# Optimization experiments

Hardware: AMD Instinct MI355X
Metric: run time of the kernel (lower is better)

Reference implementation:

```python
import jax, jax.numpy as jnp
import numpy as np

B, S, H = 32, 512, 768
NHEAD, DH = 8, 96          # 8 heads * 96 = 768
E = 4096                   # edges per sample
NC = 2
NEG = -1e9
EPS = 1e-5


def _p(k, shape, scale=0.02):
    return scale * jax.random.normal(k, shape, dtype=jnp.float32)


def setup_inputs() -> dict:
    key = jax.random.key(0)
    ks = jax.random.split(key, 24)
    z = lambda *s: jnp.zeros(s, jnp.float32)
    return {
        "diff_encoded": jax.random.normal(ks[0], (B, S, H), jnp.float32),
        "msg_encoded": jax.random.normal(ks[1], (B, S, H), jnp.float32),
        "msg_mask": jnp.ones((B, S), jnp.int32),
        "edge_index_diff": jax.random.randint(ks[2], (B, 2, E), 0, S),
        "edge_index_msg": jax.random.randint(ks[3], (B, 2, E), 0, S),
        # GATv2Conv(heads=1): lin_l (source/message), lin_r (target), att vector, output bias
        "gat_wl": _p(ks[4], (H, H)), "gat_bl": z(H),
        "gat_wr": _p(ks[5], (H, H)), "gat_br": z(H),
        "gat_att": _p(ks[6], (H,)), "gat_bias": z(H),
        # cross MultiheadAttention
        "wq": _p(ks[7], (H, H)), "bq": z(H),
        "wk": _p(ks[8], (H, H)), "bk": z(H),
        "wv": _p(ks[9], (H, H)), "bv": z(H),
        "wo": _p(ks[10], (H, H)), "bo": z(H),
        # LayerNorm + MLP head
        "ln_g": jnp.ones((H,), jnp.float32), "ln_b": z(H),
        "fc0_w": _p(ks[11], (H, 512)), "fc0_b": z(512),
        "fc1_w": _p(ks[12], (512, 128)), "fc1_b": z(128),
        "fc2_w": _p(ks[13], (128, NC)), "fc2_b": z(NC),
    }


def _gat_single(x, edges, wl, bl, wr, br, att, bias):
    # GATv2Conv, heads=1, add_self_loops=True. x: [N,H], edges: [2,E] (src, dst).
    N = x.shape[0]
    src, dst = edges[0], edges[1]
    valid = (src < N) & (dst < N)            # clip_edge_index, as a mask
    src = jnp.where(valid, src, 0)
    dst = jnp.where(valid, dst, 0)
    loop = jnp.arange(N, dtype=src.dtype)    # PyG adds self loops
    src_a = jnp.concatenate([src, loop])
    dst_a = jnp.concatenate([dst, loop])
    valid_a = jnp.concatenate([valid, jnp.ones((N,), bool)])
    xl = x @ wl + bl                          # source / message transform
    xr = x @ wr + br                          # target transform
    e = jax.nn.leaky_relu(xl[src_a] + xr[dst_a], 0.2) @ att   # [E+N]
    e = jnp.where(valid_a, e, NEG)
    emax = jax.ops.segment_max(e, dst_a, num_segments=N)
    p = jnp.exp(e - emax[dst_a]) * valid_a.astype(x.dtype)
    denom = jax.ops.segment_sum(p, dst_a, num_segments=N)
    alpha = p / denom[dst_a]
    out = jax.ops.segment_sum(alpha[:, None] * xl[src_a], dst_a, num_segments=N)
    return out + bias


_gat = jax.vmap(_gat_single, in_axes=(0, 0) + (None,) * 6)


def _layernorm(x, g, b):
    mu = jnp.mean(x, -1, keepdims=True)
    var = jnp.mean(jnp.square(x - mu), -1, keepdims=True)
    return (x - mu) * jax.lax.rsqrt(var + EPS) * g + b


def reference(diff_encoded, msg_encoded, msg_mask, edge_index_diff, edge_index_msg,
              gat_wl, gat_bl, gat_wr, gat_br, gat_att, gat_bias,
              wq, bq, wk, bk, wv, bv, wo, bo, ln_g, ln_b,
              fc0_w, fc0_b, fc1_w, fc1_b, fc2_w, fc2_b):
    diff_g = _gat(diff_encoded, edge_index_diff, gat_wl, gat_bl, gat_wr, gat_br, gat_att, gat_bias) + diff_encoded
    msg_g = _gat(msg_encoded, edge_index_msg, gat_wl, gat_bl, gat_wr, gat_br, gat_att, gat_bias) + msg_encoded
    # cross attention: query=diff_g, key/value=msg_g, key_padding_mask = (msg_mask == 0)
    q = (diff_g @ wq + bq).reshape(B, S, NHEAD, DH)
    k = (msg_g @ wk + bk).reshape(B, S, NHEAD, DH)
    v = (msg_g @ wv + bv).reshape(B, S, NHEAD, DH)
    scores = jnp.einsum("bqhd,bkhd->bhqk", q, k) / jnp.sqrt(jnp.float32(DH))
    scores = jnp.where((msg_mask == 0)[:, None, None, :], NEG, scores)
    attn = jax.nn.softmax(scores, axis=-1)
    ctx = jnp.einsum("bhqk,bkhd->bqhd", attn, v).reshape(B, S, H) @ wo + bo
    fused = _layernorm(ctx + diff_g, ln_g, ln_b)
    x = fused[:, 0, :]                                  # CLS token
    x = jax.nn.relu(x @ fc0_w + fc0_b)                  # dropout = identity (eval)
    x = jax.nn.relu(x @ fc1_w + fc1_b)
    return x @ fc2_w + fc2_b
```

## Files before the change

kernel.cpp:

```cpp
#include <hip/hip_runtime.h>
#include <hip/hip_bf16.h>
#include <math.h>

#define BB 32
#define SS 512
#define HH 768
#define NHEADC 8
#define DHC 96
#define EE 4096
#define EAC (EE + SS)
#define NCC 2
#define CAPC 128
#define CAP2 32
#define GSL 36
#define XRS 1536
#define NEGV -1000000000.0f
#define EPSV 1e-5f

typedef __hip_bfloat16 bf16;
typedef __bf16 bf16x8 __attribute__((ext_vector_type(8)));
typedef float f32x4 __attribute__((ext_vector_type(4)));

static __device__ inline unsigned short f2bf_u(float f) {
  __hip_bfloat16 h = __float2bfloat16(f);
  return *(unsigned short*)&h;
}
static __device__ inline float bfu(unsigned short u) {
  return __uint_as_float(((unsigned int)u) << 16);
}
static __device__ inline float bf2f(bf16 h) { return __bfloat162float(h); }

static __device__ inline void gload16(const void* g, void* l) {
  __builtin_amdgcn_global_load_lds(
      (const __attribute__((address_space(1))) void*)g,
      (__attribute__((address_space(3))) void*)l, 16, 0, 0);
}

__global__ __launch_bounds__(256) void k_cvt_bf16(const float* __restrict__ x,
                                                  bf16* __restrict__ y, int n) {
  int i = (blockIdx.x * 256 + threadIdx.x) * 4;
  if (i >= n) return;
  float4 v = *(const float4*)(x + i);
  ushort4 o;
  o.x = f2bf_u(v.x); o.y = f2bf_u(v.y); o.z = f2bf_u(v.z); o.w = f2bf_u(v.w);
  *(ushort4*)((unsigned short*)y + i) = o;
}

__global__ __launch_bounds__(256) void k_cvt_wt(
    const float* __restrict__ w0, const float* __restrict__ w1,
    const float* __restrict__ w2, const float* __restrict__ w3,
    bf16* __restrict__ o0, bf16* __restrict__ o1,
    bf16* __restrict__ o2, bf16* __restrict__ o3) {
  const float* w; bf16* o;
  switch (blockIdx.z) {
    case 0: w = w0; o = o0; break;
    case 1: w = w1; o = o1; break;
    case 2: w = w2; o = o2; break;
    default: w = w3; o = o3; break;
  }
  __shared__ float t[32][33];
  int n0 = blockIdx.x * 32, k0 = blockIdx.y * 32;
  int x = threadIdx.x & 31, y = threadIdx.x >> 5;
  for (int yy = y; yy < 32; yy += 8)
    t[yy][x] = w[(size_t)(k0 + yy) * HH + n0 + x];
  __syncthreads();
  for (int yy = y; yy < 32; yy += 8)
    o[(size_t)(n0 + yy) * HH + k0 + x] = __float2bfloat16(t[x][yy]);
}

__global__ __launch_bounds__(256) void k_bias_stack(
    const float* __restrict__ bl, const float* __restrict__ br,
    const float* __restrict__ bk, const float* __restrict__ bv,
    float* __restrict__ biasA, float* __restrict__ biasB) {
  int t = blockIdx.x * 256 + threadIdx.x;
  if (t < HH) {
    biasA[t] = bl[t]; biasA[HH + t] = br[t];
    biasB[t] = bk[t]; biasB[HH + t] = bv[t];
  }
}

template <typename OT>
__global__ __launch_bounds__(256) void k_gemm(
    const bf16* __restrict__ A, const bf16* __restrict__ Bt,
    const float* __restrict__ bias, OT* __restrict__ C,
    int M, int N, int K, int ldc)
{
  __shared__ __align__(16) bf16 As[128 * 32];
  __shared__ __align__(16) bf16 Bs[128 * 32];
  const int tid = threadIdx.x;
  const int wv = tid >> 6, lane = tid & 63;
  const int bm = blockIdx.x * 128, bn = blockIdx.y * 128;
  const int wm = (wv & 1) * 64, wn = (wv >> 1) * 64;
  const int m16 = lane & 15, half = lane >> 4;
  f32x4 acc[4][4];
  #pragma unroll
  for (int i = 0; i < 4; ++i)
    #pragma unroll
    for (int j = 0; j < 4; ++j) acc[i][j] = (f32x4){0.f, 0.f, 0.f, 0.f};

  const int c0 = tid, c1 = tid + 256;
  const int r0 = c0 >> 2, o0 = (c0 & 3) * 8;
  const int r1 = c1 >> 2, o1 = (c1 & 3) * 8;
  const size_t aB0 = (size_t)(bm + r0) * K + o0;
  const size_t aB1 = (size_t)(bm + r1) * K + o1;
  const size_t bB0 = (size_t)(bn + r0) * K + o0;
  const size_t bB1 = (size_t)(bn + r1) * K + o1;

  for (int k0 = 0; k0 < K; k0 += 32) {
    __syncthreads();
    gload16(A + aB0 + k0, As + (size_t)c0 * 8);
    gload16(A + aB1 + k0, As + (size_t)c1 * 8);
    gload16(Bt + bB0 + k0, Bs + (size_t)c0 * 8);
    gload16(Bt + bB1 + k0, Bs + (size_t)c1 * 8);
    __syncthreads();
    bf16x8 af[4], bfv[4];
    #pragma unroll
    for (int t = 0; t < 4; ++t) {
      af[t]  = *(const bf16x8*)(As + (wm + t * 16 + m16) * 32 + half * 8);
      bfv[t] = *(const bf16x8*)(Bs + (wn + t * 16 + m16) * 32 + half * 8);
    }
    #pragma unroll
    for (int i = 0; i < 4; ++i)
      #pragma unroll
      for (int j = 0; j < 4; ++j)
        acc[i][j] = __builtin_amdgcn_mfma_f32_16x16x32_bf16(af[i], bfv[j], acc[i][j], 0, 0, 0);
  }
  #pragma unroll
  for (int i = 0; i < 4; ++i) {
    #pragma unroll
    for (int j = 0; j < 4; ++j) {
      int col = bn + wn + j * 16 + m16;
      float bv = bias ? bias[col] : 0.f;
      #pragma unroll
      for (int r = 0; r < 4; ++r) {
        int row = bm + wm + i * 16 + half * 4 + r;
        float v = acc[i][j][r] + bv;
        if constexpr (sizeof(OT) == 2)
          C[(size_t)row * ldc + col] = (OT)__float2bfloat16(v);
        else
          C[(size_t)row * ldc + col] = v;
      }
    }
  }
}

__global__ __launch_bounds__(256) void k_gat_edge(
    const int* __restrict__ eidx, const bf16* __restrict__ xlr,
    const float* __restrict__ att,
    float* __restrict__ evals, int* __restrict__ esrc, int* __restrict__ edst,
    int* __restrict__ cnt)
{
  int w = blockIdx.x * 4 + (threadIdx.x >> 6);
  int lane = threadIdx.x & 63;
  if (w >= BB * EAC) return;
  int b = w / EAC, j = w - b * EAC;
  int s, d; bool valid;
  if (j < EE) {
    s = eidx[b * 2 * EE + j];
    d = eidx[b * 2 * EE + EE + j];
    valid = (s >= 0 && s < SS && d >= 0 && d < SS);
    if (!valid) { s = 0; d = 0; }
  } else { s = j - EE; d = s; valid = true; }
  const ushort4* pl4 = (const ushort4*)(xlr + ((size_t)b * SS + s) * XRS);
  const ushort4* pr4 = (const ushort4*)(xlr + ((size_t)b * SS + d) * XRS + HH);
  const float4* a4 = (const float4*)att;
  float part = 0.f;
  #pragma unroll
  for (int r = 0; r < 3; ++r) {
    int c = lane + 64 * r;
    ushort4 vl = pl4[c];
    ushort4 vr = pr4[c];
    float4 av = a4[c];
    float t0 = bfu(vl.x) + bfu(vr.x);
    float t1 = bfu(vl.y) + bfu(vr.y);
    float t2 = bfu(vl.z) + bfu(vr.z);
    float t3 = bfu(vl.w) + bfu(vr.w);
    t0 = t0 > 0.f ? t0 : 0.2f * t0;
    t1 = t1 > 0.f ? t1 : 0.2f * t1;
    t2 = t2 > 0.f ? t2 : 0.2f * t2;
    t3 = t3 > 0.f ? t3 : 0.2f * t3;
    part += t0 * av.x + t1 * av.y + t2 * av.z + t3 * av.w;
  }
  #pragma unroll
  for (int off = 32; off > 0; off >>= 1) part += __shfl_xor(part, off);
  if (lane == 0) {
    evals[w] = valid ? part : NEGV;
    esrc[w] = s;
    edst[w] = d;
    atomicAdd(&cnt[b * SS + d], 1);
  }
}

__global__ __launch_bounds__(512) void k_scan(const int* __restrict__ cnt,
                                              int* __restrict__ offs,
                                              int* __restrict__ cursor) {
  __shared__ int tmp[SS];
  int b = blockIdx.x, t = threadIdx.x;
  int x = cnt[b * SS + t];
  tmp[t] = x;
  __syncthreads();
  for (int off = 1; off < SS; off <<= 1) {
    int u = (t >= off) ? tmp[t - off] : 0;
    __syncthreads();
    tmp[t] += u;
    __syncthreads();
  }
  int ex = tmp[t] - x;
  offs[b * SS + t] = ex;
  cursor[b * SS + t] = ex;
}

__global__ void k_scatter(const int* __restrict__ edst, int* __restrict__ cursor,
                          int* __restrict__ binned) {
  int i = blockIdx.x * blockDim.x + threadIdx.x;
  if (i >= BB * EAC) return;
  int b = i / EAC, j = i - b * EAC;
  int d = edst[i];
  int pos = atomicAdd(&cursor[b * SS + d], 1);
  binned[b * EAC + pos] = j;
}

__global__ __launch_bounds__(64) void k_gat_reduce(
    const float* __restrict__ evals, const int* __restrict__ esrc,
    const int* __restrict__ binned, const int* __restrict__ offs,
    const int* __restrict__ cnt, const bf16* __restrict__ xlr,
    const float* __restrict__ gbias, const float* __restrict__ resid,
    bf16* __restrict__ out)
{
  int b = blockIdx.x / SS, d = blockIdx.x % SS;
  int lane = threadIdx.x;
  int base = offs[b * SS + d], n = cnt[b * SS + d];
  const float* ev = evals + (size_t)b * EAC;
  const int* bb = binned + (size_t)b * EAC + base;
  float m = -3.0e38f;
  for (int i = lane; i < n; i += 64) m = fmaxf(m, ev[bb[i]]);
  #pragma unroll
  for (int off = 32; off > 0; off >>= 1) m = fmaxf(m, __shfl_xor(m, off));
  float ssum = 0.f;
  for (int i = lane; i < n; i += 64) ssum += expf(ev[bb[i]] - m);
  #pragma unroll
  for (int off = 32; off > 0; off >>= 1) ssum += __shfl_xor(ssum, off);
  float inv = 1.f / ssum;
  float acc[12] = {};
  for (int i = 0; i < n; ++i) {
    int j = bb[i];
    float a = expf(ev[j] - m) * inv;
    const ushort4* px4 =
        (const ushort4*)(xlr + ((size_t)b * SS + esrc[(size_t)b * EAC + j]) * XRS);
    #pragma unroll
    for (int r = 0; r < 3; ++r) {
      ushort4 v = px4[lane + 64 * r];
      acc[4 * r + 0] += a * bfu(v.x);
      acc[4 * r + 1] += a * bfu(v.y);
      acc[4 * r + 2] += a * bfu(v.z);
      acc[4 * r + 3] += a * bfu(v.w);
    }
  }
  size_t o = ((size_t)b * SS + d) * HH;
  const float4* gb4 = (const float4*)gbias;
  const float4* rs4 = (const float4*)(resid + o);
  ushort4* out4 = (ushort4*)(out + o);
  #pragma unroll
  for (int r = 0; r < 3; ++r) {
    int c = lane + 64 * r;
    float4 g = gb4[c], rr = rs4[c];
    ushort4 ov;
    ov.x = f2bf_u(acc[4 * r + 0] + g.x + rr.x);
    ov.y = f2bf_u(acc[4 * r + 1] + g.y + rr.y);
    ov.z = f2bf_u(acc[4 * r + 2] + g.z + rr.z);
    ov.w = f2bf_u(acc[4 * r + 3] + g.w + rr.w);
    out4[c] = ov;
  }
}

__global__ void k_diff_collect(const int* __restrict__ eidx, int* __restrict__ dcnt,
                               int* __restrict__ dsrc) {
  int i = blockIdx.x * blockDim.x + threadIdx.x;
  if (i >= BB * EAC) return;
  int b = i / EAC, j = i - b * EAC;
  int s, d; bool valid;
  if (j < EE) {
    s = eidx[b * 2 * EE + j];
    d = eidx[b * 2 * EE + EE + j];
    valid = (s >= 0 && s < SS && d >= 0 && d < SS);
  } else { s = j - EE; d = s; valid = true; }
  if (valid && d == 0) {
    int pos = atomicAdd(&dcnt[b], 1);
    if (pos < CAPC) dsrc[b * CAPC + pos] = s;
  }
}

__global__ __launch_bounds__(192) void k_gather_diff(
    const int* __restrict__ dcnt, const int* __restrict__ dsrc,
    const float* __restrict__ diff_enc, bf16* __restrict__ G)
{
  int b = blockIdx.y, jj = blockIdx.x;
  int n = min(dcnt[b], CAP2);
  int t = threadIdx.x;
  size_t orow = ((size_t)b * GSL + jj) * HH;
  ushort4 o = {0, 0, 0, 0};
  if (jj < n || jj == CAP2) {
    int s = (jj == CAP2) ? 0 : dsrc[b * CAPC + jj];
    float4 v = ((const float4*)(diff_enc + ((size_t)b * SS + s) * HH))[t];
    o.x = f2bf_u(v.x); o.y = f2bf_u(v.y); o.z = f2bf_u(v.z); o.w = f2bf_u(v.w);
  }
  *(ushort4*)((unsigned short*)G + orow + t * 4) = o;
}

__global__ __launch_bounds__(256) void k_diff_gat0(
    const int* __restrict__ dcnt, const float* __restrict__ GD,
    const float* __restrict__ att, const float* __restrict__ gbias,
    const float* __restrict__ diff_enc, float* __restrict__ dg0)
{
  int b = blockIdx.x;
  int n = min(dcnt[b], CAP2);
  __shared__ float ee[CAP2];
  __shared__ float al[CAP2];
  __shared__ float xr0s[HH];
  int wave = threadIdx.x >> 6, lane = threadIdx.x & 63;
  for (int h = threadIdx.x; h < HH; h += 256)
    xr0s[h] = GD[((size_t)b * GSL + CAP2) * XRS + HH + h];
  __syncthreads();
  for (int jj = wave; jj < n; jj += 4) {
    const float* px = GD + ((size_t)b * GSL + jj) * XRS;
    float part = 0.f;
    #pragma unroll
    for (int r = 0; r < HH / 64; ++r) {
      int h = lane + 64 * r;
      float t = px[h] + xr0s[h];
      t = t > 0.f ? t : 0.2f * t;
      part += t * att[h];
    }
    #pragma unroll
    for (int off = 32; off > 0; off >>= 1) part += __shfl_xor(part, off);
    if (lane == 0) ee[jj] = part;
  }
  __syncthreads();
  if (threadIdx.x == 0) {
    float m = -3.0e38f;
    for (int i = 0; i < n; ++i) m = fmaxf(m, ee[i]);
    float ssum = 0.f;
    for (int i = 0; i < n; ++i) ssum += expf(ee[i] - m);
    float inv = 1.f / ssum;
    for (int i = 0; i < n; ++i) al[i] = expf(ee[i] - m) * inv;
  }
  __syncthreads();
  for (int h = threadIdx.x; h < HH; h += 256) {
    float acc = 0.f;
    for (int i = 0; i < n; ++i) acc += al[i] * GD[((size_t)b * GSL + i) * XRS + h];
    dg0[b * HH + h] = acc + gbias[h] + diff_enc[(size_t)b * SS * HH + h];
  }
}

__global__ __launch_bounds__(256) void k_colmat(
    const float* __restrict__ in, const float* __restrict__ w,
    const float* __restrict__ bias, const float* __restrict__ extra,
    float* __restrict__ outp, int Kd, int Nd, long in_stride, int relu)
{
  int b = blockIdx.y, n0 = blockIdx.x * 64;
  int tid = threadIdx.x, wv = tid >> 6, lane = tid & 63;
  __shared__ float xs[HH];
  __shared__ float red[4][64];
  const float* src = in + (size_t)b * in_stride;
  for (int k = tid; k < Kd; k += 256) xs[k] = src[k];
  __syncthreads();
  int h = n0 + lane;
  int kpw = Kd >> 2;
  int kb = wv * kpw;
  float acc = 0.f;
  for (int k = 0; k < kpw; k += 8) {
    #pragma unroll
    for (int u = 0; u < 8; ++u) {
      int kk = kb + k + u;
      acc += xs[kk] * w[(size_t)kk * Nd + h];
    }
  }
  red[wv][lane] = acc;
  __syncthreads();
  if (tid < 64) {
    float s = red[0][tid] + red[1][tid] + red[2][tid] + red[3][tid] + bias[n0 + tid];
    if (extra) s += extra[(size_t)b * Nd + n0 + tid];
    if (relu) s = fmaxf(s, 0.f);
    outp[(size_t)b * Nd + n0 + tid] = s;
  }
}

__global__ __launch_bounds__(256) void k_ln(
    const float* __restrict__ xin, const float* __restrict__ g,
    const float* __restrict__ bta, float* __restrict__ yout)
{
  int b = blockIdx.x, tid = threadIdx.x;
  __shared__ float red[4], redq[4];
  float v0 = xin[b * HH + tid];
  float v1 = xin[b * HH + tid + 256];
  float v2 = xin[b * HH + tid + 512];
  float sum = v0 + v1 + v2;
  float sq = v0 * v0 + v1 * v1 + v2 * v2;
  #pragma unroll
  for (int off = 32; off > 0; off >>= 1) { sum += __shfl_xor(sum, off); sq += __shfl_xor(sq, off); }
  int wv = tid >> 6, lane = tid & 63;
  if (lane == 0) { red[wv] = sum; redq[wv] = sq; }
  __syncthreads();
  sum = red[0] + red[1] + red[2] + red[3];
  sq = redq[0] + redq[1] + redq[2] + redq[3];
  float mu = sum / HH;
  float var = sq / HH - mu * mu;
  float scl = rsqrtf(var + EPSV);
  yout[b * HH + tid]       = (v0 - mu) * scl * g[tid]       + bta[tid];
  yout[b * HH + tid + 256] = (v1 - mu) * scl * g[tid + 256] + bta[tid + 256];
  yout[b * HH + tid + 512] = (v2 - mu) * scl * g[tid + 512] + bta[tid + 512];
}

__global__ __launch_bounds__(256) void k_fc12(
    const float* __restrict__ a0g, const float* __restrict__ fc1w,
    const float* __restrict__ fc1b, const float* __restrict__ fc2w,
    const float* __restrict__ fc2b, float* __restrict__ out)
{
  int b = blockIdx.x, tid = threadIdx.x;
  __shared__ float a0s[512];
  __shared__ float a1s[128];
  __shared__ float r1[2][128];
  for (int k = tid; k < 512; k += 256) a0s[k] = a0g[b * 512 + k];
  __syncthreads();
  int o = tid & 127, hf = tid >> 7;
  int kb = hf * 256;
  float acc = 0.f;
  for (int k = 0; k < 256; k += 8) {
    #pragma unroll
    for (int u = 0; u < 8; ++u) {
      int kk = kb + k + u;
      acc += a0s[kk] * fc1w[(size_t)kk * 128 + o];
    }
  }
  r1[hf][o] = acc;
  __syncthreads();
  if (tid < 128) a1s[tid] = fmaxf(r1[0][tid] + r1[1][tid] + fc1b[tid], 0.f);
  __syncthreads();
  if (tid < 128) {
    int oo = tid >> 6, l = tid & 63;
    float p = a1s[l] * fc2w[l * 2 + oo] + a1s[l + 64] * fc2w[(l + 64) * 2 + oo];
    #pragma unroll
    for (int off = 32; off > 0; off >>= 1) p += __shfl_xor(p, off);
    if (l == 0) out[b * NCC + oo] = p + fc2b[oo];
  }
}

__global__ __launch_bounds__(512) void k_attn(
    const float* __restrict__ q0, const bf16* __restrict__ kvb,
    const int* __restrict__ mask, float* __restrict__ ctx)
{
  int b = blockIdx.x / NHEADC, hd = blockIdx.x % NHEADC;
  __shared__ float qs[DHC];
  __shared__ float sc[SS];
  __shared__ float redm[8];
  __shared__ float reds[8];
  __shared__ float pr4[4][DHC];
  int tid = threadIdx.x;
  if (tid < DHC) qs[tid] = q0[b * HH + hd * DHC + tid];
  __syncthreads();
  const float scale = 0.10206207261596575f;
  {
    int s = tid;
    const int4* pk4 = (const int4*)(kvb + ((size_t)b * SS + s) * XRS + hd * DHC);
    float acc = 0.f;
    #pragma unroll
    for (int c = 0; c < 12; ++c) {
      int4 raw = pk4[c];
      const unsigned short* u = (const unsigned short*)&raw;
      #pragma unroll
      for (int j = 0; j < 8; ++j) acc += qs[c * 8 + j] * bfu(u[j]);
    }
    sc[s] = (mask[b * SS + s] != 0) ? acc * scale : NEGV;
  }
  __syncthreads();
  int wave = tid >> 6, lane = tid & 63;
  float m = sc[tid];
  #pragma unroll
  for (int off = 32; off > 0; off >>= 1) m = fmaxf(m, __shfl_xor(m, off));
  if (lane == 0) redm[wave] = m;
  __syncthreads();
  m = redm[0];
  #pragma unroll
  for (int i = 1; i < 8; ++i) m = fmaxf(m, redm[i]);
  float p0 = expf(sc[tid] - m);
  float ssum = p0;
  #pragma unroll
  for (int off = 32; off > 0; off >>= 1) ssum += __shfl_xor(ssum, off);
  if (lane == 0) reds[wave] = ssum;
  __syncthreads();
  ssum = reds[0] + reds[1] + reds[2] + reds[3] + reds[4] + reds[5] + reds[6] + reds[7];
  float inv = 1.f / ssum;
  sc[tid] = p0 * inv;
  __syncthreads();
  {
    int hs = tid >> 7, d = tid & 127;
    if (d < DHC) {
      const bf16* pv = kvb + ((size_t)b * SS + hs * 128) * XRS + HH + hd * DHC + d;
      float acc = 0.f;
      for (int s = 0; s < 128; s += 8) {
        #pragma unroll
        for (int u = 0; u < 8; ++u)
          acc += sc[hs * 128 + s + u] * bf2f(pv[(size_t)(s + u) * XRS]);
      }
      pr4[hs][d] = acc;
    }
  }
  __syncthreads();
  if (tid < DHC)
    ctx[b * HH + hd * DHC + tid] = pr4[0][tid] + pr4[1][tid] + pr4[2][tid] + pr4[3][tid];
}

extern "C" void kernel_launch(void* const* d_in, const int* in_sizes, int n_in,
                              void* d_out, int out_size, void* d_ws, size_t ws_size,
                              hipStream_t stream) {
  const float* diff_enc = (const float*)d_in[0];
  const float* msg_enc  = (const float*)d_in[1];
  const int*   msg_mask = (const int*)d_in[2];
  const int*   e_diff   = (const int*)d_in[3];
  const int*   e_msg    = (const int*)d_in[4];
  const float* gat_wl   = (const float*)d_in[5];
  const float* gat_bl   = (const float*)d_in[6];
  const float* gat_wr   = (const float*)d_in[7];
  const float* gat_br   = (const float*)d_in[8];
  const float* gat_att  = (const float*)d_in[9];
  const float* gat_bias = (const float*)d_in[10];
  const float* wq = (const float*)d_in[11];
  const float* bq = (const float*)d_in[12];
  const float* wk = (const float*)d_in[13];
  const float* bk = (const float*)d_in[14];
  const float* wv = (const float*)d_in[15];
  const float* bv = (const float*)d_in[16];
  const float* wo = (const float*)d_in[17];
  const float* bo = (const float*)d_in[18];
  const float* ln_g = (const float*)d_in[19];
  const float* ln_b = (const float*)d_in[20];
  const float* fc0w = (const float*)d_in[21];
  const float* fc0b = (const float*)d_in[22];
  const float* fc1w = (const float*)d_in[23];
  const float* fc1b = (const float*)d_in[24];
  const float* fc2w = (const float*)d_in[25];
  const float* fc2b = (const float*)d_in[26];
  float* out = (float*)d_out;

  char* ws = (char*)d_ws;
  size_t off = 0;
  auto alloc = [&](size_t bytes) -> void* {
    void* p = (void*)(ws + off);
    off += (bytes + 255) & ~(size_t)255;
    return p;
  };
  bf16* Abf    = (bf16*)alloc((size_t)BB * SS * HH * 2);
  bf16* xlr    = (bf16*)alloc((size_t)BB * SS * XRS * 2);
  bf16* kv     = (bf16*)alloc((size_t)BB * SS * XRS * 2);
  bf16* mg     = (bf16*)alloc((size_t)BB * SS * HH * 2);
  bf16* wtA    = (bf16*)alloc((size_t)2 * HH * HH * 2);
  bf16* wtB    = (bf16*)alloc((size_t)2 * HH * HH * 2);
  float* biasA = (float*)alloc((size_t)XRS * 4);
  float* biasB = (float*)alloc((size_t)XRS * 4);
  float* ev    = (float*)alloc((size_t)BB * EAC * 4);
  int*   esrc  = (int*)alloc((size_t)BB * EAC * 4);
  int*   edst  = (int*)alloc((size_t)BB * EAC * 4);
  int*   cnt   = (int*)alloc((size_t)BB * SS * 4);
  int*   offs  = (int*)alloc((size_t)BB * SS * 4);
  int*   cursor= (int*)alloc((size_t)BB * SS * 4);
  int*   binned= (int*)alloc((size_t)BB * EAC * 4);
  bf16*  G     = (bf16*)alloc((size_t)BB * GSL * HH * 2);
  float* GD    = (float*)alloc((size_t)BB * GSL * XRS * 4);
  int*   dcnt  = (int*)alloc((size_t)BB * 4);
  int*   dsrc  = (int*)alloc((size_t)BB * CAPC * 4);
  float* dg0   = (float*)alloc((size_t)BB * HH * 4);
  float* q0    = (float*)alloc((size_t)BB * HH * 4);
  float* ctx   = (float*)alloc((size_t)BB * HH * 4);
  float* fpre  = (float*)alloc((size_t)BB * HH * 4);
  float* fnrm  = (float*)alloc((size_t)BB * HH * 4);
  float* a0g   = (float*)alloc((size_t)BB * 512 * 4);

  hipMemsetAsync(cnt, 0, (size_t)BB * SS * 4, stream);
  hipMemsetAsync(dcnt, 0, (size_t)BB * 4, stream);

  const int nA = BB * SS * HH;
  k_cvt_bf16<<<nA / 1024, 256, 0, stream>>>(msg_enc, Abf, nA);
  dim3 wtGrid(HH / 32, HH / 32, 4);
  k_cvt_wt<<<wtGrid, 256, 0, stream>>>(gat_wl, gat_wr, wk, wv,
                                       wtA, wtA + (size_t)HH * HH,
                                       wtB, wtB + (size_t)HH * HH);
  k_bias_stack<<<3, 256, 0, stream>>>(gat_bl, gat_br, bk, bv, biasA, biasB);

  dim3 gBlk(256), gGridA((BB * SS) / 128, XRS / 128);
  k_gemm<bf16><<<gGridA, gBlk, 0, stream>>>(Abf, wtA, biasA, xlr,
                                            BB * SS, XRS, HH, XRS);
  k_gat_edge<<<(BB * EAC) / 4, 256, 0, stream>>>(e_msg, xlr, gat_att,
                                                 ev, esrc, edst, cnt);
  k_scan<<<BB, SS, 0, stream>>>(cnt, offs, cursor);
  k_scatter<<<(BB * EAC + 255) / 256, 256, 0, stream>>>(edst, cursor, binned);
  k_gat_reduce<<<BB * SS, 64, 0, stream>>>(ev, esrc, binned, offs, cnt, xlr,
                                           gat_bias, msg_enc, mg);
  k_gemm<bf16><<<gGridA, gBlk, 0, stream>>>(mg, wtB, biasB, kv,
                                            BB * SS, XRS, HH, XRS);
  k_diff_collect<<<(BB * EAC + 255) / 256, 256, 0, stream>>>(e_diff, dcnt, dsrc);
  {
    dim3 gg(GSL, BB);
    k_gather_diff<<<gg, 192, 0, stream>>>(dcnt, dsrc, diff_enc, G);
    dim3 gGridD((BB * GSL) / 128, XRS / 128);
    k_gemm<float><<<gGridD, gBlk, 0, stream>>>(G, wtA, biasA, GD,
                                               BB * GSL, XRS, HH, XRS);
  }
  k_diff_gat0<<<BB, 256, 0, stream>>>(dcnt, GD, gat_att, gat_bias, diff_enc, dg0);
  {
    dim3 g(HH / 64, BB);
    k_colmat<<<g, 256, 0, stream>>>(dg0, wq, bq, nullptr, q0, HH, HH, HH, 0);
  }
  k_attn<<<BB * NHEADC, 512, 0, stream>>>(q0, kv, msg_mask, ctx);
  {
    dim3 g(HH / 64, BB);
    k_colmat<<<g, 256, 0, stream>>>(ctx, wo, bo, dg0, fpre, HH, HH, HH, 0);
  }
  k_ln<<<BB, 256, 0, stream>>>(fpre, ln_g, ln_b, fnrm);
  {
    dim3 g(512 / 64, BB);
    k_colmat<<<g, 256, 0, stream>>>(fnrm, fc0w, fc0b, nullptr, a0g, HH, 512, HH, 1);
  }
  k_fc12<<<BB, 256, 0, stream>>>(a0g, fc1w, fc1b, fc2w, fc2b, out);
}
```

Before: 511.5 us.

## Fuse GAT edge scoring into per-destination online-softmax aggregation

Removes the separate per-edge scoring kernel and its evals/esrc/edst buffers. Each destination node's wave now computes edge logits on the fly, using the target row it loaded once, and accumulates with an online softmax. The edge counting and binning now read the raw edge index directly, and the diff-graph collection is merged into the same counting kernel. The binning is moved ahead of the first GEMM. The cost is a serial wave-wide reduction per edge inside the aggregation loop, and a change in the order of entries in dsrc.

After: 469.4 us. 1.09x faster.

```diff
diff --git a/kernel.cpp b/kernel.cpp
--- a/kernel.cpp
+++ b/kernel.cpp
@@ -8,7 +8,6 @@
 #define NHEADC 8
 #define DHC 96
 #define EE 4096
-#define EAC (EE + SS)
 #define NCC 2
 #define CAPC 128
 #define CAP2 32
@@ -144,50 +143,24 @@
   }
 }
 
-__global__ __launch_bounds__(256) void k_gat_edge(
-    const int* __restrict__ eidx, const bf16* __restrict__ xlr,
-    const float* __restrict__ att,
-    float* __restrict__ evals, int* __restrict__ esrc, int* __restrict__ edst,
-    int* __restrict__ cnt)
-{
-  int w = blockIdx.x * 4 + (threadIdx.x >> 6);
-  int lane = threadIdx.x & 63;
-  if (w >= BB * EAC) return;
-  int b = w / EAC, j = w - b * EAC;
-  int s, d; bool valid;
-  if (j < EE) {
-    s = eidx[b * 2 * EE + j];
-    d = eidx[b * 2 * EE + EE + j];
-    valid = (s >= 0 && s < SS && d >= 0 && d < SS);
-    if (!valid) { s = 0; d = 0; }
-  } else { s = j - EE; d = s; valid = true; }
-  const ushort4* pl4 = (const ushort4*)(xlr + ((size_t)b * SS + s) * XRS);
-  const ushort4* pr4 = (const ushort4*)(xlr + ((size_t)b * SS + d) * XRS + HH);
-  const float4* a4 = (const float4*)att;
-  float part = 0.f;
-  #pragma unroll
-  for (int r = 0; r < 3; ++r) {
-    int c = lane + 64 * r;
-    ushort4 vl = pl4[c];
-    ushort4 vr = pr4[c];
-    float4 av = a4[c];
-    float t0 = bfu(vl.x) + bfu(vr.x);
-    float t1 = bfu(vl.y) + bfu(vr.y);
-    float t2 = bfu(vl.z) + bfu(vr.z);
-    float t3 = bfu(vl.w) + bfu(vr.w);
-    t0 = t0 > 0.f ? t0 : 0.2f * t0;
-    t1 = t1 > 0.f ? t1 : 0.2f * t1;
-    t2 = t2 > 0.f ? t2 : 0.2f * t2;
-    t3 = t3 > 0.f ? t3 : 0.2f * t3;
-    part += t0 * av.x + t1 * av.y + t2 * av.z + t3 * av.w;
-  }
-  #pragma unroll
-  for (int off = 32; off > 0; off >>= 1) part += __shfl_xor(part, off);
-  if (lane == 0) {
-    evals[w] = valid ? part : NEGV;
-    esrc[w] = s;
-    edst[w] = d;
+__global__ __launch_bounds__(256) void k_count2(
+    const int* __restrict__ e_msg, const int* __restrict__ e_diff,
+    int* __restrict__ cnt, int* __restrict__ dcnt, int* __restrict__ dsrc)
+{
+  int i = blockIdx.x * blockDim.x + threadIdx.x;
+  if (i >= BB * EE) return;
+  int b = i / EE, j = i - b * EE;
+  int s = e_msg[b * 2 * EE + j], d = e_msg[b * 2 * EE + EE + j];
+  if (s >= 0 && s < SS && d >= 0 && d < SS)
     atomicAdd(&cnt[b * SS + d], 1);
+  int s2 = e_diff[b * 2 * EE + j], d2 = e_diff[b * 2 * EE + EE + j];
+  if (s2 >= 0 && s2 < SS && d2 == 0) {
+    int pos = atomicAdd(&dcnt[b], 1);
+    if (pos < CAPC) dsrc[b * CAPC + pos] = s2;
+  }
+  if (j == 0) {
+    int pos = atomicAdd(&dcnt[b], 1);
+    if (pos < CAPC) dsrc[b * CAPC + pos] = 0;
   }
 }
 
@@ -210,52 +183,76 @@
   cursor[b * SS + t] = ex;
 }
 
-__global__ void k_scatter(const int* __restrict__ edst, int* __restrict__ cursor,
+__global__ void k_scatter(const int* __restrict__ e_msg, int* __restrict__ cursor,
                           int* __restrict__ binned) {
   int i = blockIdx.x * blockDim.x + threadIdx.x;
-  if (i >= BB * EAC) return;
-  int b = i / EAC, j = i - b * EAC;
-  int d = edst[i];
-  int pos = atomicAdd(&cursor[b * SS + d], 1);
-  binned[b * EAC + pos] = j;
-}
-
-__global__ __launch_bounds__(64) void k_gat_reduce(
-    const float* __restrict__ evals, const int* __restrict__ esrc,
+  if (i >= BB * EE) return;
+  int b = i / EE, j = i - b * EE;
+  int s = e_msg[b * 2 * EE + j], d = e_msg[b * 2 * EE + EE + j];
+  if (s >= 0 && s < SS && d >= 0 && d < SS) {
+    int pos = atomicAdd(&cursor[b * SS + d], 1);
+    binned[(size_t)b * EE + pos] = s;
+  }
+}
+
+__global__ __launch_bounds__(256) void k_gat_fused(
     const int* __restrict__ binned, const int* __restrict__ offs,
     const int* __restrict__ cnt, const bf16* __restrict__ xlr,
-    const float* __restrict__ gbias, const float* __restrict__ resid,
-    bf16* __restrict__ out)
-{
-  int b = blockIdx.x / SS, d = blockIdx.x % SS;
-  int lane = threadIdx.x;
+    const float* __restrict__ att, const float* __restrict__ gbias,
+    const float* __restrict__ resid, bf16* __restrict__ out)
+{
+  int g = blockIdx.x * 4 + (threadIdx.x >> 6);
+  int lane = threadIdx.x & 63;
+  int b = g / SS, d = g - b * SS;
   int base = offs[b * SS + d], n = cnt[b * SS + d];
-  const float* ev = evals + (size_t)b * EAC;
-  const int* bb = binned + (size_t)b * EAC + base;
-  float m = -3.0e38f;
-  for (int i = lane; i < n; i += 64) m = fmaxf(m, ev[bb[i]]);
-  #pragma unroll
-  for (int off = 32; off > 0; off >>= 1) m = fmaxf(m, __shfl_xor(m, off));
-  float ssum = 0.f;
-  for (int i = lane; i < n; i += 64) ssum += expf(ev[bb[i]] - m);
-  #pragma unroll
-  for (int off = 32; off > 0; off >>= 1) ssum += __shfl_xor(ssum, off);
-  float inv = 1.f / ssum;
+  const int* bin = binned + (size_t)b * EE + base;
+  float av[12];
+  {
+    const float4* a4 = (const float4*)att;
+    #pragma unroll
+    for (int r = 0; r < 3; ++r) {
+      float4 t = a4[lane + 64 * r];
+      av[4*r] = t.x; av[4*r+1] = t.y; av[4*r+2] = t.z; av[4*r+3] = t.w;
+    }
+  }
+  float xr[12];
+  {
+    const ushort4* p = (const ushort4*)(xlr + ((size_t)b * SS + d) * XRS + HH);
+    #pragma unroll
+    for (int r = 0; r < 3; ++r) {
+      ushort4 v = p[lane + 64 * r];
+      xr[4*r] = bfu(v.x); xr[4*r+1] = bfu(v.y); xr[4*r+2] = bfu(v.z); xr[4*r+3] = bfu(v.w);
+    }
+  }
+  float m = -3.0e38f, l = 0.f;
   float acc[12] = {};
-  for (int i = 0; i < n; ++i) {
-    int j = bb[i];
-    float a = expf(ev[j] - m) * inv;
-    const ushort4* px4 =
-        (const ushort4*)(xlr + ((size_t)b * SS + esrc[(size_t)b * EAC + j]) * XRS);
+  for (int i = -1; i < n; ++i) {
+    int s = (i < 0) ? d : bin[i];
+    float xs[12];
+    const ushort4* p = (const ushort4*)(xlr + ((size_t)b * SS + s) * XRS);
     #pragma unroll
     for (int r = 0; r < 3; ++r) {
-      ushort4 v = px4[lane + 64 * r];
-      acc[4 * r + 0] += a * bfu(v.x);
-      acc[4 * r + 1] += a * bfu(v.y);
-      acc[4 * r + 2] += a * bfu(v.z);
-      acc[4 * r + 3] += a * bfu(v.w);
-    }
-  }
+      ushort4 v = p[lane + 64 * r];
+      xs[4*r] = bfu(v.x); xs[4*r+1] = bfu(v.y); xs[4*r+2] = bfu(v.z); xs[4*r+3] = bfu(v.w);
+    }
+    float e = 0.f;
+    #pragma unroll
+    for (int k = 0; k < 12; ++k) {
+      float t = xs[k] + xr[k];
+      t = t > 0.f ? t : 0.2f * t;
+      e += t * av[k];
+    }
+    #pragma unroll
+    for (int off = 32; off > 0; off >>= 1) e += __shfl_xor(e, off);
+    float mn = fmaxf(m, e);
+    float so = __expf(m - mn);
+    float w  = __expf(e - mn);
+    l = l * so + w;
+    #pragma unroll
+    for (int k = 0; k < 12; ++k) acc[k] = acc[k] * so + w * xs[k];
+    m = mn;
+  }
+  float inv = 1.f / l;
   size_t o = ((size_t)b * SS + d) * HH;
   const float4* gb4 = (const float4*)gbias;
   const float4* rs4 = (const float4*)(resid + o);
@@ -263,30 +260,13 @@
   #pragma unroll
   for (int r = 0; r < 3; ++r) {
     int c = lane + 64 * r;
-    float4 g = gb4[c], rr = rs4[c];
+    float4 gg = gb4[c], rr = rs4[c];
     ushort4 ov;
-    ov.x = f2bf_u(acc[4 * r + 0] + g.x + rr.x);
-    ov.y = f2bf_u(acc[4 * r + 1] + g.y + rr.y);
-    ov.z = f2bf_u(acc[4 * r + 2] + g.z + rr.z);
-    ov.w = f2bf_u(acc[4 * r + 3] + g.w + rr.w);
+    ov.x = f2bf_u(acc[4*r+0] * inv + gg.x + rr.x);
+    ov.y = f2bf_u(acc[4*r+1] * inv + gg.y + rr.y);
+    ov.z = f2bf_u(acc[4*r+2] * inv + gg.z + rr.z);
+    ov.w = f2bf_u(acc[4*r+3] * inv + gg.w + rr.w);
     out4[c] = ov;
-  }
-}
-
-__global__ void k_diff_collect(const int* __restrict__ eidx, int* __restrict__ dcnt,
-                               int* __restrict__ dsrc) {
-  int i = blockIdx.x * blockDim.x + threadIdx.x;
-  if (i >= BB * EAC) return;
-  int b = i / EAC, j = i - b * EAC;
-  int s, d; bool valid;
-  if (j < EE) {
-    s = eidx[b * 2 * EE + j];
-    d = eidx[b * 2 * EE + EE + j];
-    valid = (s >= 0 && s < SS && d >= 0 && d < SS);
-  } else { s = j - EE; d = s; valid = true; }
-  if (valid && d == 0) {
-    int pos = atomicAdd(&dcnt[b], 1);
-    if (pos < CAPC) dsrc[b * CAPC + pos] = s;
   }
 }
 
@@ -557,13 +537,10 @@
   bf16* wtB    = (bf16*)alloc((size_t)2 * HH * HH * 2);
   float* biasA = (float*)alloc((size_t)XRS * 4);
   float* biasB = (float*)alloc((size_t)XRS * 4);
-  float* ev    = (float*)alloc((size_t)BB * EAC * 4);
-  int*   esrc  = (int*)alloc((size_t)BB * EAC * 4);
-  int*   edst  = (int*)alloc((size_t)BB * EAC * 4);
   int*   cnt   = (int*)alloc((size_t)BB * SS * 4);
   int*   offs  = (int*)alloc((size_t)BB * SS * 4);
   int*   cursor= (int*)alloc((size_t)BB * SS * 4);
-  int*   binned= (int*)alloc((size_t)BB * EAC * 4);
+  int*   binned= (int*)alloc((size_t)BB * EE * 4);
   bf16*  G     = (bf16*)alloc((size_t)BB * GSL * HH * 2);
   float* GD    = (float*)alloc((size_t)BB * GSL * XRS * 4);
   int*   dcnt  = (int*)alloc((size_t)BB * 4);
@@ -586,18 +563,17 @@
                                        wtB, wtB + (size_t)HH * HH);
   k_bias_stack<<<3, 256, 0, stream>>>(gat_bl, gat_br, bk, bv, biasA, biasB);
 
+  k_count2<<<(BB * EE + 255) / 256, 256, 0, stream>>>(e_msg, e_diff, cnt, dcnt, dsrc);
+  k_scan<<<BB, SS, 0, stream>>>(cnt, offs, cursor);
+  k_scatter<<<(BB * EE + 255) / 256, 256, 0, stream>>>(e_msg, cursor, binned);
+
   dim3 gBlk(256), gGridA((BB * SS) / 128, XRS / 128);
   k_gemm<bf16><<<gGridA, gBlk, 0, stream>>>(Abf, wtA, biasA, xlr,
                                             BB * SS, XRS, HH, XRS);
-  k_gat_edge<<<(BB * EAC) / 4, 256, 0, stream>>>(e_msg, xlr, gat_att,
-                                                 ev, esrc, edst, cnt);
-  k_scan<<<BB, SS, 0, stream>>>(cnt, offs, cursor);
-  k_scatter<<<(BB * EAC + 255) / 256, 256, 0, stream>>>(edst, cursor, binned);
-  k_gat_reduce<<<BB * SS, 64, 0, stream>>>(ev, esrc, binned, offs, cnt, xlr,
-                                           gat_bias, msg_enc, mg);
+  k_gat_fused<<<(BB * SS) / 4, 256, 0, stream>>>(binned, offs, cnt, xlr,
+                                                 gat_att, gat_bias, msg_enc, mg);
   k_gemm<bf16><<<gGridA, gBlk, 0, stream>>>(mg, wtB, biasB, kv,
                                             BB * SS, XRS, HH, XRS);
-  k_diff_collect<<<(BB * EAC + 255) / 256, 256, 0, stream>>>(e_diff, dcnt, dsrc);
   {
     dim3 gg(GSL, BB);
     k_gather_diff<<<gg, 192, 0, stream>>>(dcnt, dsrc, diff_enc, G);
```
